# Optimization experiments

Measured on AMD Instinct MI355X. Metric: run time of the kernel, lower is better.

## Reference

```python
import jax, jax.numpy as jnp
import numpy as np

NUM_HEADS = 16

def alibi_slopes(num_heads):
    # 1 / ((2**8)**(1/H))**(i+1) for i in range(H)  -> shape (H, 1, 1)
    x = (2.0 ** 8) ** (1.0 / num_heads)
    return (1.0 / x ** (jnp.arange(1, num_heads + 1, dtype=jnp.float32)))[:, None, None]

def setup_inputs() -> dict:
    key = jax.random.key(0)
    k1, k2, k3 = jax.random.split(key, 3)
    B, T, D = 4, 2048, 1024
    x = jax.random.normal(k1, (B, T, D), dtype=jnp.float32)
    w_qkv = jax.random.normal(k2, (D, 3 * D), dtype=jnp.float32) * 0.02
    w_o = jax.random.normal(k3, (D, D), dtype=jnp.float32) * 0.02
    return {"x": x, "w_qkv": w_qkv, "w_o": w_o}

def reference(x, w_qkv, w_o):
    B, T, C = x.shape
    H = NUM_HEADS
    dh = C // H
    qkv = x @ w_qkv                                   # [B, T, 3C]
    q, k, v = jnp.split(qkv, 3, axis=-1)
    # b t (h d) -> b h t d
    q = q.reshape(B, T, H, dh).transpose(0, 2, 1, 3)
    k = k.reshape(B, T, H, dh).transpose(0, 2, 1, 3)
    v = v.reshape(B, T, H, dh).transpose(0, 2, 1, 3)
    wei = jnp.einsum('bhqd,bhkd->bhqk', q, k)         # [B, H, T, T]
    rel = (jnp.arange(T)[None, :] - jnp.arange(T)[:, None]).astype(jnp.float32)
    bias = alibi_slopes(H) * rel                      # [H, T, T]
    scale = jnp.float32(C) ** 0.5                     # note: full dim C, as in source
    scores = wei / scale + bias
    causal = jnp.tril(jnp.ones((T, T), dtype=bool))
    scores = jnp.where(causal, scores, jnp.float32(-jnp.inf))
    attn = jax.nn.softmax(scores, axis=-1)
    out = jnp.einsum('bhqk,bhkd->bhqd', attn, v)      # [B, H, T, dh]
    concat = out.transpose(0, 2, 1, 3).reshape(B, T, C)
    return concat @ w_o
```

## Files before the change

kernel.cpp:

```cpp
#include <hip/hip_runtime.h>
#include <hip/hip_bf16.h>

typedef float f32x4 __attribute__((ext_vector_type(4)));
typedef short bf16x8 __attribute__((ext_vector_type(8)));
typedef short bf16x4 __attribute__((ext_vector_type(4)));

static __device__ __forceinline__ short f2bs(float f) {
  __hip_bfloat16 h = __float2bfloat16(f);
  union { __hip_bfloat16 h; short s; } u;
  u.h = h;
  return u.s;
}

#define GLDS(gp, lp) __builtin_amdgcn_global_load_lds( \
    (const __attribute__((address_space(1))) unsigned int*)(gp), \
    (__attribute__((address_space(3))) unsigned int*)(lp), 16, 0, 0)

__global__ __launch_bounds__(256) void cvt_f32_bf16(const float* __restrict__ in,
                                                    short* __restrict__ out, int n4) {
  int i = blockIdx.x * 256 + threadIdx.x;
  if (i >= n4) return;
  f32x4 v = ((const f32x4*)in)[i];
  bf16x4 o;
  o[0] = f2bs(v[0]); o[1] = f2bs(v[1]); o[2] = f2bs(v[2]); o[3] = f2bs(v[3]);
  ((bf16x4*)out)[i] = o;
}

__global__ __launch_bounds__(256) void transpose_cvt(const float* __restrict__ in,
                                                     short* __restrict__ out,
                                                     int R, int C) {
  __shared__ float tile[32][33];
  int bx = blockIdx.x * 32;
  int by = blockIdx.y * 32;
  int tx = threadIdx.x & 31;
  int ty = threadIdx.x >> 5;
#pragma unroll
  for (int i = 0; i < 32; i += 8)
    tile[ty + i][tx] = in[(long)(by + ty + i) * C + bx + tx];
  __syncthreads();
#pragma unroll
  for (int i = 0; i < 32; i += 8)
    out[(long)(bx + ty + i) * R + by + tx] = f2bs(tile[tx][ty + i]);
}

__device__ __forceinline__ void gemm_compute_tile(const short* Ac, const short* Bc,
                                                  int r0, int c0, int lr, int quad,
                                                  f32x4 acc[4][4]) {
  bf16x8 af[4], bfr[4];
#pragma unroll
  for (int i = 0; i < 4; ++i)
    af[i] = *(const bf16x8*)(Ac + (r0 + i * 16 + lr) * 32 + quad * 8);
#pragma unroll
  for (int j = 0; j < 4; ++j)
    bfr[j] = *(const bf16x8*)(Bc + (c0 + j * 16 + lr) * 32 + quad * 8);
#pragma unroll
  for (int i = 0; i < 4; ++i)
#pragma unroll
    for (int j = 0; j < 4; ++j)
      acc[i][j] = __builtin_amdgcn_mfma_f32_16x16x32_bf16(af[i], bfr[j], acc[i][j], 0, 0, 0);
}

__device__ __forceinline__ void gemm_mainloop(const short* __restrict__ A,
                                              const short* __restrict__ Bt,
                                              int K, int rowA0, int rowB0,
                                              short* As, short* Bs,
                                              f32x4 acc[4][4]) {
  const int tid = threadIdx.x;
  const int wave = tid >> 6;
  const int lane = tid & 63;
  const int lr = lane & 15;
  const int quad = lane >> 4;
  const short* aP = A + (long)(rowA0 + wave * 32 + (lane >> 2)) * K + (lane & 3) * 8;
  const short* bP = Bt + (long)(rowB0 + wave * 32 + (lane >> 2)) * K + (lane & 3) * 8;
  const int woff = wave * 32 * 32;
  const int r0 = (wave >> 1) * 64;
  const int c0 = (wave & 1) * 64;
  const int c16K = 16 * K;
  const int BUF = 128 * 32;
  GLDS(aP, As + woff);
  GLDS(aP + c16K, As + woff + 16 * 32);
  GLDS(bP, Bs + woff);
  GLDS(bP + c16K, Bs + woff + 16 * 32);
  aP += 32; bP += 32;
  const int nIter = K >> 5;
#pragma unroll 1
  for (int i = 0; i < nIter; i += 2) {
    __syncthreads();
    if (i + 1 < nIter) {
      GLDS(aP, As + BUF + woff);
      GLDS(aP + c16K, As + BUF + woff + 16 * 32);
      GLDS(bP, Bs + BUF + woff);
      GLDS(bP + c16K, Bs + BUF + woff + 16 * 32);
      aP += 32; bP += 32;
    }
    gemm_compute_tile(As, Bs, r0, c0, lr, quad, acc);
    __syncthreads();
    if (i + 2 < nIter) {
      GLDS(aP, As + woff);
      GLDS(aP + c16K, As + woff + 16 * 32);
      GLDS(bP, Bs + woff);
      GLDS(bP + c16K, Bs + woff + 16 * 32);
      aP += 32; bP += 32;
    }
    gemm_compute_tile(As + BUF, Bs + BUF, r0, c0, lr, quad, acc);
  }
}

__global__ __launch_bounds__(256, 5) void gemm_qkv(const short* __restrict__ xb,
                                                   const short* __restrict__ wT,
                                                   short* __restrict__ q,
                                                   short* __restrict__ k,
                                                   short* __restrict__ vt) {
  __shared__ __align__(16) short As[2 * 128 * 32];
  __shared__ __align__(16) short Bs[2 * 128 * 32];
  f32x4 acc[4][4];
#pragma unroll
  for (int i = 0; i < 4; ++i)
#pragma unroll
    for (int j = 0; j < 4; ++j)
      acc[i][j] = (f32x4){0.f, 0.f, 0.f, 0.f};
  const int tileM = blockIdx.x * 128;
  const int tileN = blockIdx.y * 128;
  gemm_mainloop(xb, wT, 1024, tileM, tileN, As, Bs, acc);
  const int tid = threadIdx.x;
  const int wave = tid >> 6;
  const int lane = tid & 63;
  const int lr = lane & 15;
  const int quad = lane >> 4;
  const int wrow = wave >> 1;
  const int wcol = wave & 1;
#pragma unroll
  for (int i = 0; i < 4; ++i) {
    const int row0 = tileM + wrow * 64 + i * 16 + quad * 4;
    const int b = row0 >> 11;
    const int t = row0 & 2047;
#pragma unroll
    for (int j = 0; j < 4; ++j) {
      int col = tileN + wcol * 64 + j * 16 + lr;
      int region = col >> 10;
      int w = col & 1023;
      int h = w >> 6;
      int d = w & 63;
      long bh = (long)b * 16 + h;
      if (region == 0) {
#pragma unroll
        for (int r = 0; r < 4; ++r)
          q[(bh * 2048 + t + r) * 64 + d] = f2bs(acc[i][j][r] * 0.03125f);
      } else if (region == 1) {
#pragma unroll
        for (int r = 0; r < 4; ++r)
          k[(bh * 2048 + t + r) * 64 + d] = f2bs(acc[i][j][r]);
      } else {
        bf16x4 pk;
#pragma unroll
        for (int r = 0; r < 4; ++r) pk[r] = f2bs(acc[i][j][r]);
        *(bf16x4*)(vt + (bh * 64 + d) * 2048 + t) = pk;
      }
    }
  }
}

__global__ __launch_bounds__(256, 5) void attn(const short* __restrict__ q,
                                               const short* __restrict__ kk,
                                               const short* __restrict__ vt,
                                               short* __restrict__ cat) {
  __shared__ __align__(16) short Ks[64 * 72];
  __shared__ __align__(16) short Vs[64 * 72];
  __shared__ __align__(16) short Ps[4 * 16 * 72];
  const int bx = blockIdx.x;
  const int g = bx >> 8;
  const int hshift = ((g & 1) << 3) | ((g & 2) << 1) | ((g & 4) >> 1);
  const int j = 31 - (bx >> 6);
  const int bh = (bx + hshift) & 63;
  const int h = bh & 15;
  const int b = bh >> 4;
  const int tid = threadIdx.x;
  const int wave = tid >> 6;
  const int lane = tid & 63;
  const int lr = lane & 15;
  const int quad = lane >> 4;
  const float l2e = 1.44269504f;
  const float slope = exp2f(-0.5f * (float)(h + 1));
  const float slope_l2e = slope * l2e;
  const float c2 = -2.0f * l2e;
  const int d_cut = (int)ceilf(20.0f * exp2f(0.5f * (float)(h + 1)));
  const short* kbg = kk + (long)bh * 2048 * 64;
  const short* vbg = vt + (long)bh * 64 * 2048;
  const int srow = tid >> 3;
  const int scol = (tid & 7) * 8;
  short* pw = Ps + wave * 16 * 72;

  const int q0 = j * 64;
  const int mrow0 = q0 + wave * 16;
  const int kt_start = max(0, (q0 - d_cut) >> 6);
  const short* qptr = q + ((long)bh * 2048 + mrow0) * 64;
  bf16x8 qf0 = *(const bf16x8*)(qptr + (long)lr * 64 + quad * 8);
  bf16x8 qf1 = *(const bf16x8*)(qptr + (long)lr * 64 + 32 + quad * 8);
  float lp = 0.f;
  f32x4 O[4];
#pragma unroll
  for (int dt = 0; dt < 4; ++dt) O[dt] = (f32x4){0.f, 0.f, 0.f, 0.f};
  float bias[4][4];
  unsigned okbits = 0;
#pragma unroll
  for (int ct = 0; ct < 4; ++ct)
#pragma unroll
    for (int r = 0; r < 4; ++r) {
      int off = ct * 16 + quad * 4 + r;
      bias[ct][r] = slope_l2e * (float)(kt_start * 64 + off - mrow0 - lr) + c2;
      if (off - wave * 16 - lr <= 0) okbits |= 1u << (ct * 4 + r);
    }
  const float bstep = slope_l2e * 64.0f;

  const short* kg = kbg + (long)kt_start * 64 * 64;
  const short* vg = vbg + kt_start * 64;
  bf16x8 pk0 = *(const bf16x8*)(kg + srow * 64 + scol);
  bf16x8 pk1 = *(const bf16x8*)(kg + (srow + 32) * 64 + scol);
  bf16x8 pv0 = *(const bf16x8*)(vg + (long)srow * 2048 + scol);
  bf16x8 pv1 = *(const bf16x8*)(vg + (long)(srow + 32) * 2048 + scol);
  for (int kt = kt_start; kt <= j; ++kt) {
    *(bf16x8*)(Ks + srow * 72 + scol) = pk0;
    *(bf16x8*)(Ks + (srow + 32) * 72 + scol) = pk1;
    *(bf16x8*)(Vs + srow * 72 + scol) = pv0;
    *(bf16x8*)(Vs + (srow + 32) * 72 + scol) = pv1;
    __syncthreads();
    if (kt < j) {
      const short* kg2 = kbg + (long)(kt + 1) * 64 * 64;
      const short* vg2 = vbg + (kt + 1) * 64;
      pk0 = *(const bf16x8*)(kg2 + srow * 64 + scol);
      pk1 = *(const bf16x8*)(kg2 + (srow + 32) * 64 + scol);
      pv0 = *(const bf16x8*)(vg2 + (long)srow * 2048 + scol);
      pv1 = *(const bf16x8*)(vg2 + (long)(srow + 32) * 2048 + scol);
    }
    f32x4 S[4];
    __builtin_amdgcn_s_setprio(1);
#pragma unroll
    for (int ct = 0; ct < 4; ++ct) {
      bf16x8 kf0 = *(const bf16x8*)(Ks + (ct * 16 + lr) * 72 + quad * 8);
      bf16x8 kf1 = *(const bf16x8*)(Ks + (ct * 16 + lr) * 72 + 32 + quad * 8);
      f32x4 a = (f32x4){0.f, 0.f, 0.f, 0.f};
      a = __builtin_amdgcn_mfma_f32_16x16x32_bf16(kf0, qf0, a, 0, 0, 0);
      a = __builtin_amdgcn_mfma_f32_16x16x32_bf16(kf1, qf1, a, 0, 0, 0);
      S[ct] = a;
    }
    __builtin_amdgcn_s_setprio(0);
    const bool diag = (kt == j);
#pragma unroll
    for (int ct = 0; ct < 4; ++ct) {
      bf16x4 pkt;
#pragma unroll
      for (int r = 0; r < 4; ++r) {
        float arg = fmaf(S[ct][r], l2e, bias[ct][r]);
        if (diag && !(okbits & (1u << (ct * 4 + r)))) arg = -10000.0f;
        float p = exp2f(arg);
        lp += p;
        pkt[r] = f2bs(p);
        bias[ct][r] += bstep;
      }
      *(bf16x4*)(pw + lr * 72 + ct * 16 + quad * 4) = pkt;
    }
    asm volatile("s_waitcnt lgkmcnt(0)" ::: "memory");
    bf16x8 pf0 = *(const bf16x8*)(pw + lr * 72 + quad * 8);
    bf16x8 pf1 = *(const bf16x8*)(pw + lr * 72 + 32 + quad * 8);
    __builtin_amdgcn_s_setprio(1);
#pragma unroll
    for (int dt = 0; dt < 4; ++dt) {
      bf16x8 vf0 = *(const bf16x8*)(Vs + (dt * 16 + lr) * 72 + quad * 8);
      bf16x8 vf1 = *(const bf16x8*)(Vs + (dt * 16 + lr) * 72 + 32 + quad * 8);
      O[dt] = __builtin_amdgcn_mfma_f32_16x16x32_bf16(pf0, vf0, O[dt], 0, 0, 0);
      O[dt] = __builtin_amdgcn_mfma_f32_16x16x32_bf16(pf1, vf1, O[dt], 0, 0, 0);
    }
    __builtin_amdgcn_s_setprio(0);
    __syncthreads();
  }
  lp += __shfl_xor(lp, 16);
  lp += __shfl_xor(lp, 32);
#pragma unroll
  for (int r = 0; r < 4; ++r) {
    float lm = __shfl(lp, quad * 4 + r);
    float inv = 1.0f / lm;
    int t = mrow0 + quad * 4 + r;
#pragma unroll
    for (int dt = 0; dt < 4; ++dt)
      cat[((long)b * 2048 + t) * 1024 + h * 64 + dt * 16 + lr] =
          f2bs(O[dt][r] * inv);
  }
}

__global__ __launch_bounds__(256, 5) void gemm_out(const short* __restrict__ cat,
                                                   const short* __restrict__ woT,
                                                   float* __restrict__ out) {
  __shared__ __align__(16) short As[2 * 128 * 32];
  __shared__ __align__(16) short Bs[2 * 128 * 32];
  f32x4 acc[4][4];
#pragma unroll
  for (int i = 0; i < 4; ++i)
#pragma unroll
    for (int j = 0; j < 4; ++j)
      acc[i][j] = (f32x4){0.f, 0.f, 0.f, 0.f};
  const int tileM = blockIdx.x * 128;
  const int tileN = blockIdx.y * 128;
  gemm_mainloop(cat, woT, 1024, tileM, tileN, As, Bs, acc);
  const int tid = threadIdx.x;
  const int wave = tid >> 6;
  const int lane = tid & 63;
  const int lr = lane & 15;
  const int quad = lane >> 4;
#pragma unroll
  for (int i = 0; i < 4; ++i)
#pragma unroll
    for (int j = 0; j < 4; ++j) {
      int col = tileN + (wave & 1) * 64 + j * 16 + lr;
#pragma unroll
      for (int r = 0; r < 4; ++r) {
        int row = tileM + (wave >> 1) * 64 + i * 16 + quad * 4 + r;
        out[(long)row * 1024 + col] = acc[i][j][r];
      }
    }
}

extern "C" void kernel_launch(void* const* d_in, const int* in_sizes, int n_in,
                              void* d_out, int out_size, void* d_ws, size_t ws_size,
                              hipStream_t stream) {
  const float* x = (const float*)d_in[0];
  const float* w_qkv = (const float*)d_in[1];
  const float* w_o = (const float*)d_in[2];
  float* out = (float*)d_out;
  short* ws = (short*)d_ws;
  short* xb = ws;
  short* wqkvT = xb + 8388608;
  short* woT = wqkvT + 3145728;
  short* q = woT + 1048576;
  short* kb = q + 8388608;
  short* vt = kb + 8388608;

  cvt_f32_bf16<<<8192, 256, 0, stream>>>(x, xb, 2097152);
  transpose_cvt<<<dim3(96, 32), 256, 0, stream>>>(w_qkv, wqkvT, 1024, 3072);
  transpose_cvt<<<dim3(32, 32), 256, 0, stream>>>(w_o, woT, 1024, 1024);
  gemm_qkv<<<dim3(64, 24), 256, 0, stream>>>(xb, wqkvT, q, kb, vt);
  attn<<<dim3(2048), 256, 0, stream>>>(q, kb, vt, xb );
  gemm_out<<<dim3(64, 8), 256, 0, stream>>>(xb, woT, out);
}
```

Baseline: 246.4 us.

## Merge prep kernels into one launch and XOR-swizzle GEMM LDS tiles

Folds the x conversion and the two weight transpose-convert kernels into a single prep kernel that picks its role from the block index, removing two kernel launches. It also applies an XOR swizzle to the 16-byte chunk positions used by the global-to-LDS loads in the GEMM mainloop, with a matching inverse swizzle on the LDS fragment reads, to reduce LDS bank conflicts. The swizzle must stay consistent between writer and reader lanes or the results will be wrong.

```diff
diff --git a/kernel.cpp b/kernel.cpp
--- a/kernel.cpp
+++ b/kernel.cpp
@@ -16,24 +16,34 @@
     (const __attribute__((address_space(1))) unsigned int*)(gp), \
     (__attribute__((address_space(3))) unsigned int*)(lp), 16, 0, 0)
 
-__global__ __launch_bounds__(256) void cvt_f32_bf16(const float* __restrict__ in,
-                                                    short* __restrict__ out, int n4) {
-  int i = blockIdx.x * 256 + threadIdx.x;
-  if (i >= n4) return;
-  f32x4 v = ((const f32x4*)in)[i];
-  bf16x4 o;
-  o[0] = f2bs(v[0]); o[1] = f2bs(v[1]); o[2] = f2bs(v[2]); o[3] = f2bs(v[3]);
-  ((bf16x4*)out)[i] = o;
-}
-
-__global__ __launch_bounds__(256) void transpose_cvt(const float* __restrict__ in,
-                                                     short* __restrict__ out,
-                                                     int R, int C) {
+__global__ __launch_bounds__(256) void prep(const float* __restrict__ x,
+                                            const float* __restrict__ w_qkv,
+                                            const float* __restrict__ w_o,
+                                            short* __restrict__ xb,
+                                            short* __restrict__ wqkvT,
+                                            short* __restrict__ woT) {
   __shared__ float tile[32][33];
-  int bx = blockIdx.x * 32;
-  int by = blockIdx.y * 32;
-  int tx = threadIdx.x & 31;
-  int ty = threadIdx.x >> 5;
+  const int bid = blockIdx.x;
+  if (bid < 8192) {
+    int i = bid * 256 + threadIdx.x;
+    f32x4 v = ((const f32x4*)x)[i];
+    bf16x4 o;
+    o[0] = f2bs(v[0]); o[1] = f2bs(v[1]); o[2] = f2bs(v[2]); o[3] = f2bs(v[3]);
+    ((bf16x4*)xb)[i] = o;
+    return;
+  }
+  const float* in; short* out; int R, C, bx, by;
+  if (bid < 11264) {
+    int b2 = bid - 8192;
+    in = w_qkv; out = wqkvT; R = 1024; C = 3072;
+    bx = (b2 % 96) * 32; by = (b2 / 96) * 32;
+  } else {
+    int b3 = bid - 11264;
+    in = w_o; out = woT; R = 1024; C = 1024;
+    bx = (b3 % 32) * 32; by = (b3 / 32) * 32;
+  }
+  const int tx = threadIdx.x & 31;
+  const int ty = threadIdx.x >> 5;
 #pragma unroll
   for (int i = 0; i < 32; i += 8)
     tile[ty + i][tx] = in[(long)(by + ty + i) * C + bx + tx];
@@ -46,13 +56,14 @@
 __device__ __forceinline__ void gemm_compute_tile(const short* Ac, const short* Bc,
                                                   int r0, int c0, int lr, int quad,
                                                   f32x4 acc[4][4]) {
+  const int rq = (quad ^ ((lr >> 1) & 3)) * 8;
   bf16x8 af[4], bfr[4];
 #pragma unroll
   for (int i = 0; i < 4; ++i)
-    af[i] = *(const bf16x8*)(Ac + (r0 + i * 16 + lr) * 32 + quad * 8);
+    af[i] = *(const bf16x8*)(Ac + (r0 + i * 16 + lr) * 32 + rq);
 #pragma unroll
   for (int j = 0; j < 4; ++j)
-    bfr[j] = *(const bf16x8*)(Bc + (c0 + j * 16 + lr) * 32 + quad * 8);
+    bfr[j] = *(const bf16x8*)(Bc + (c0 + j * 16 + lr) * 32 + rq);
 #pragma unroll
   for (int i = 0; i < 4; ++i)
 #pragma unroll
@@ -70,8 +81,9 @@
   const int lane = tid & 63;
   const int lr = lane & 15;
   const int quad = lane >> 4;
-  const short* aP = A + (long)(rowA0 + wave * 32 + (lane >> 2)) * K + (lane & 3) * 8;
-  const short* bP = Bt + (long)(rowB0 + wave * 32 + (lane >> 2)) * K + (lane & 3) * 8;
+  const int swz = ((lane & 3) ^ ((lane >> 3) & 3)) * 8;
+  const short* aP = A + (long)(rowA0 + wave * 32 + (lane >> 2)) * K + swz;
+  const short* bP = Bt + (long)(rowB0 + wave * 32 + (lane >> 2)) * K + swz;
   const int woff = wave * 32 * 32;
   const int r0 = (wave >> 1) * 64;
   const int c0 = (wave & 1) * 64;
@@ -334,9 +346,7 @@
   short* kb = q + 8388608;
   short* vt = kb + 8388608;
 
-  cvt_f32_bf16<<<8192, 256, 0, stream>>>(x, xb, 2097152);
-  transpose_cvt<<<dim3(96, 32), 256, 0, stream>>>(w_qkv, wqkvT, 1024, 3072);
-  transpose_cvt<<<dim3(32, 32), 256, 0, stream>>>(w_o, woT, 1024, 1024);
+  prep<<<12288, 256, 0, stream>>>(x, w_qkv, w_o, xb, wqkvT, woT);
   gemm_qkv<<<dim3(64, 24), 256, 0, stream>>>(xb, wqkvT, q, kb, vt);
   attn<<<dim3(2048), 256, 0, stream>>>(q, kb, vt, xb );
   gemm_out<<<dim3(64, 8), 256, 0, stream>>>(xb, woT, out);
```

New measurement: 247.2 us. No clear change (+0.3%).
